# Kernel tuning notes

Hardware: AMD Instinct MI355X
Metric: run time of the kernel (lower is better)

## Reference

```python
import jax, jax.numpy as jnp
import numpy as np
from jax import lax

B, N, NPOINT, NSAMPLE = 16, 8192, 2048, 32
RADIUS = 0.45
D_FEAT = 64
MLP = (64, 64, 128)
EPS = 1e-5  # BatchNorm2d default eps


def setup_inputs() -> dict:
    key = jax.random.key(0)
    ks = jax.random.split(key, 8)
    inp = {
        "xyz": jax.random.uniform(ks[0], (B, 3, N), dtype=jnp.float32),
        "points": jax.random.normal(ks[1], (B, D_FEAT, N), dtype=jnp.float32),
    }
    dims = (3 + D_FEAT,) + MLP
    for i in range(len(MLP)):
        ci, co = dims[i], dims[i + 1]
        inp[f"W{i}"] = jax.random.normal(ks[2 + i], (co, ci), dtype=jnp.float32) / np.float32(np.sqrt(ci))
        inp[f"b{i}"] = jnp.zeros((co,), jnp.float32)
        inp[f"gamma{i}"] = jnp.ones((co,), jnp.float32)
        inp[f"beta{i}"] = jnp.zeros((co,), jnp.float32)
    return inp


def _fps(xyz_t, npoint):
    # farthest point sampling; xyz_t: [B, N, 3] -> [B, npoint] indices
    Bc, Nc, _ = xyz_t.shape

    def step(carry, _):
        distance, farthest = carry
        centroid = jnp.take_along_axis(xyz_t, farthest[:, None, None], axis=1)  # [B,1,3]
        d = jnp.sum((xyz_t - centroid) ** 2, axis=-1)  # [B,N]
        distance = jnp.minimum(distance, d)
        return (distance, jnp.argmax(distance, axis=-1)), farthest

    init = (jnp.full((Bc, Nc), 1e10, xyz_t.dtype), jnp.zeros((Bc,), jnp.int32))
    _, cents = lax.scan(step, init, None, length=npoint)
    return jnp.transpose(cents)  # [B, npoint]


def _gather(pts, idx):
    # pts: [B, N, C], idx: [B, ...] -> [B, ..., C]
    return jax.vmap(lambda p, i: p[i])(pts, idx)


def _forward(xyz, points, params):
    xyz_t = jnp.transpose(xyz, (0, 2, 1))     # [B,N,3]
    pts_t = jnp.transpose(points, (0, 2, 1))  # [B,N,D]

    fps_idx = _fps(xyz_t, NPOINT)
    new_xyz = _gather(xyz_t, fps_idx)         # [B,S,3]

    # ball query -- faithful to source: Euclidean DISTANCE compared vs radius**2
    d2 = (jnp.sum(new_xyz ** 2, -1)[:, :, None]
          + jnp.sum(xyz_t ** 2, -1)[:, None, :]
          - 2.0 * jnp.einsum('bsc,bnc->bsn', new_xyz, xyz_t))
    dist = jnp.sqrt(jnp.maximum(d2, 0.0))     # [B,S,N] == torch.cdist
    neg_vals, idx = lax.top_k(-dist, NSAMPLE)
    group_idx = jnp.where(-neg_vals < RADIUS ** 2, idx, 0)  # [B,S,K]

    grouped_xyz = _gather(xyz_t, group_idx) - new_xyz[:, :, None, :]  # [B,S,K,3]
    grouped_pts = _gather(pts_t, group_idx)                           # [B,S,K,D]
    feats = jnp.concatenate([grouped_xyz, grouped_pts], axis=-1)      # [B,S,K,3+D]

    # shared MLP: 1x1 conv + BatchNorm (training-mode batch stats) + ReLU
    for (W, b, g, be) in params:
        h = jnp.einsum('bskc,oc->bsko', feats, W) + b
        mean = jnp.mean(h, axis=(0, 1, 2))
        var = jnp.var(h, axis=(0, 1, 2))  # biased, like torch BN normalization
        feats = jax.nn.relu(g * (h - mean) * lax.rsqrt(var + EPS) + be)

    new_points = jnp.max(feats, axis=2)  # max over nsample -> [B,S,C_out]
    return jnp.transpose(new_xyz, (0, 2, 1)), jnp.transpose(new_points, (0, 2, 1))


def reference(xyz, points, W0, b0, gamma0, beta0, W1, b1, gamma1, beta1, W2, b2, gamma2, beta2):
    params = [(W0, b0, gamma0, beta0), (W1, b1, gamma1, beta1), (W2, b2, gamma2, beta2)]
    return _forward(xyz, points, params)
```

## Files before the change

### kernel.cpp

```cpp
#include <hip/hip_runtime.h>

#define B_ 16
#define N_ 8192
#define S_ 2048
#define K_ 32
#define EPSBN 1e-5
#define CAP 1024

#define OFF_PARTA    0ul
#define OFF_NEWXYZ   131072ul
#define OFF_GIDX     524288ul
#define OFF_Q1       4718592ul
#define OFF_C1       38273024ul
#define OFF_PART     46661632ul
#define OFF_AFF1     55050240ul
#define OFF_AFF2     55051264ul
#define OFF_AFF3     55052288ul
#define OFF_H3MAX    55053312ul
#define OFF_H3MIN    71830528ul

#define STG(row, c) ((row)*33 + ((row)>>5) + (c))

template<int CTRL, int RM>
__device__ __forceinline__ unsigned long long dppmove(unsigned long long x) {
    unsigned int lo = (unsigned int)x, hi = (unsigned int)(x >> 32);
    unsigned int lo2 = (unsigned int)__builtin_amdgcn_update_dpp((int)lo, (int)lo, CTRL, RM, 0xf, false);
    unsigned int hi2 = (unsigned int)__builtin_amdgcn_update_dpp((int)hi, (int)hi, CTRL, RM, 0xf, false);
    return ((unsigned long long)hi2 << 32) | lo2;
}
__device__ __forceinline__ unsigned long long wave_max_u64(unsigned long long x) {
    unsigned long long t;
    t = dppmove<0x111, 0xf>(x); x = (t > x) ? t : x;
    t = dppmove<0x112, 0xf>(x); x = (t > x) ? t : x;
    t = dppmove<0x114, 0xf>(x); x = (t > x) ? t : x;
    t = dppmove<0x118, 0xf>(x); x = (t > x) ? t : x;
    t = dppmove<0x142, 0xa>(x); x = (t > x) ? t : x;
    t = dppmove<0x143, 0xc>(x); x = (t > x) ? t : x;
    return x;
}
__device__ __forceinline__ unsigned long long wave_min_u64(unsigned long long x) {
    unsigned long long t;
    t = dppmove<0x111, 0xf>(x); x = (t < x) ? t : x;
    t = dppmove<0x112, 0xf>(x); x = (t < x) ? t : x;
    t = dppmove<0x114, 0xf>(x); x = (t < x) ? t : x;
    t = dppmove<0x118, 0xf>(x); x = (t < x) ? t : x;
    t = dppmove<0x142, 0xa>(x); x = (t < x) ? t : x;
    t = dppmove<0x143, 0xc>(x); x = (t < x) ? t : x;
    return x;
}

__global__ __launch_bounds__(512) void fps_kernel(const float* __restrict__ xyz,
                                                  const float* __restrict__ pts,
                                                  const float* __restrict__ W0,
                                                  const float* __restrict__ b0,
                                                  float* __restrict__ Q1,
                                                  float* __restrict__ nxyz,
                                                  float* __restrict__ out0) {
    __shared__ float xs[N_], ys[N_], zs[N_];
    __shared__ int farHist[S_];
    __shared__ unsigned long long kq[2][8];
    int tid = threadIdx.x;
    if (blockIdx.x >= 16) {
        int o = tid & 63, jj = tid >> 6;
        int blk = blockIdx.x - 16;
        int b = blk >> 10;
        int j = ((blk & 1023) << 3) + jj;
        const float* xb = xyz + (size_t)b * 3 * N_;
        const float* pb = pts + (size_t)b * 64 * N_;
        float acc = b0[o];
#pragma unroll
        for (int c = 0; c < 3; c++) acc += W0[o * 67 + c] * xb[c * N_ + j];
#pragma unroll 8
        for (int c = 0; c < 64; c++) acc += W0[o * 67 + 3 + c] * pb[c * N_ + j];
        Q1[(((size_t)b << 13) + j) * 64 + o] = acc;
        return;
    }
    int b = blockIdx.x;
    const float* xb = xyz + (size_t)b * 3 * N_;
    for (int i = tid; i < N_; i += 512) {
        xs[i] = xb[i]; ys[i] = xb[N_ + i]; zs[i] = xb[2 * N_ + i];
    }
    __syncthreads();
    float px[16], py[16], pz[16], d8[16];
#pragma unroll
    for (int k = 0; k < 16; k++) {
        int i = tid + k * 512;
        px[k] = xs[i]; py[k] = ys[i]; pz[k] = zs[i];
        d8[k] = 1e10f;
    }
    int far = 0;
    int w = tid >> 6;
    for (int t = 0; t < S_; t++) {
        if (tid == 0) farHist[t] = far;
        float cx = xs[far], cy = ys[far], cz = zs[far];
        float bv = -1.f; int bk = 0;
#pragma unroll
        for (int k = 0; k < 16; k++) {
            float dx = px[k] - cx, dy = py[k] - cy, dz = pz[k] - cz;
            float d = dx * dx + dy * dy + dz * dz;
            float dd = fminf(d8[k], d); d8[k] = dd;
            if (dd > bv) { bv = dd; bk = k; }
        }
        int bi = tid + bk * 512;
        unsigned long long kk = (((unsigned long long)__float_as_uint(bv)) << 32)
                              | (unsigned)(8191 - bi);
        kk = wave_max_u64(kk);
        int buf = t & 1;
        if ((tid & 63) == 63) kq[buf][w] = kk;
        __syncthreads();
        unsigned long long fk = kq[buf][0];
#pragma unroll
        for (int q = 1; q < 8; q++) { unsigned long long o = kq[buf][q]; fk = (o > fk) ? o : fk; }
        far = 8191 - (int)(fk & 0xffffffffull);
    }
    __syncthreads();
    for (int s = tid; s < S_; s += 512) {
        int idx = farHist[s];
        float x = xs[idx], y = ys[idx], z = zs[idx];
        int g = b * S_ + s;
        nxyz[g * 3 + 0] = x; nxyz[g * 3 + 1] = y; nxyz[g * 3 + 2] = z;
        out0[(b * 3 + 0) * S_ + s] = x;
        out0[(b * 3 + 1) * S_ + s] = y;
        out0[(b * 3 + 2) * S_ + s] = z;
    }
}

__global__ __launch_bounds__(64) void ball_kernel(const float* __restrict__ xyz,
                                                  const float* __restrict__ nxyz,
                                                  int* __restrict__ gidx) {
    __shared__ unsigned long long keys[CAP];
    __shared__ int cnt;
    int bs = blockIdx.x; int b = bs >> 11; int tid = threadIdx.x;
    const float* xb = xyz + (size_t)b * 3 * N_;
    float cx = nxyz[bs * 3 + 0], cy = nxyz[bs * 3 + 1], cz = nxyz[bs * 3 + 2];
    float csq = __fadd_rn(__fadd_rn(__fmul_rn(cx, cx), __fmul_rn(cy, cy)), __fmul_rn(cz, cz));
    const float R2F = (float)(0.45 * 0.45);
    if (tid == 0) cnt = 0;
    __syncthreads();
    for (int j = tid; j < N_; j += 64) {
        float qx = xb[j], qy = xb[N_ + j], qz = xb[2 * N_ + j];
        float psq = __fadd_rn(__fadd_rn(__fmul_rn(qx, qx), __fmul_rn(qy, qy)), __fmul_rn(qz, qz));
        float t = __fmul_rn(cx, qx);
        t = __fmaf_rn(cy, qy, t);
        t = __fmaf_rn(cz, qz, t);
        float d2 = __fsub_rn(__fadd_rn(csq, psq), __fadd_rn(t, t));
        float dist = __fsqrt_rn(fmaxf(d2, 0.0f));
        if (dist < R2F) {
            int p = atomicAdd(&cnt, 1);
            if (p < CAP) keys[p] = (((unsigned long long)__float_as_uint(dist)) << 32) | (unsigned)j;
        }
    }
    __syncthreads();
    int nc = cnt; if (nc > CAP) nc = CAP;
    for (int k = 0; k < K_; k++) {
        unsigned long long bk = ~0ull;
        for (int i = tid; i < nc; i += 64) {
            unsigned long long kv = keys[i];
            bk = (kv < bk) ? kv : bk;
        }
        bk = wave_min_u64(bk);
        unsigned int lo = (unsigned int)__builtin_amdgcn_readlane((int)(unsigned int)bk, 63);
        unsigned int hi = (unsigned int)__builtin_amdgcn_readlane((int)(unsigned int)(bk >> 32), 63);
        unsigned long long mk = ((unsigned long long)hi << 32) | lo;
        int j = 0;
        if (mk != ~0ull) {
            j = (int)(mk & 0xffffffffull);
            for (int i = tid; i < nc; i += 64)
                if (keys[i] == mk) keys[i] = ~0ull;
        }
        if (tid == 0) gidx[bs * K_ + k] = j;
    }
}

__global__ __launch_bounds__(256) void c1_kernel(const float* __restrict__ nxyz,
                                                 const float* __restrict__ W0,
                                                 float* __restrict__ C1) {
    int tid = threadIdx.x; int o = tid & 63, ss = tid >> 6;
    int gs = blockIdx.x * 4 + ss;
    float acc = 0.f;
#pragma unroll
    for (int c = 0; c < 3; c++) acc += W0[o * 67 + c] * nxyz[gs * 3 + c];
    C1[(size_t)gs * 64 + o] = acc;
}

__global__ __launch_bounds__(256) void stats1_kernel(const float* __restrict__ Q1,
                                                     const float* __restrict__ C1,
                                                     const int* __restrict__ gidx,
                                                     double* __restrict__ part) {
    __shared__ double ds1[4][64], ds2[4][64];
    int tid = threadIdx.x; int o = tid & 63, ll = tid >> 6;
    double s1 = 0, s2 = 0;
    for (int it = 0; it < 256; it++) {
        int slot = it * 4096 + blockIdx.x * 4 + ll;
        int b = slot >> 16; int r = slot & 65535; int s = r >> 5;
        int g = gidx[slot];
        float q = Q1[(((size_t)b << 13) + g) * 64 + o];
        float c = C1[((size_t)(b << 11) + s) * 64 + o];
        float h = q - c;
        s1 += h; s2 += (double)h * (double)h;
    }
    ds1[ll][o] = s1; ds2[ll][o] = s2;
    __syncthreads();
    if (tid < 64) {
        double a = 0, bb = 0;
        for (int l = 0; l < 4; l++) { a += ds1[l][tid]; bb += ds2[l][tid]; }
        part[blockIdx.x * 256 + tid * 2] = a;
        part[blockIdx.x * 256 + tid * 2 + 1] = bb;
    }
}

__global__ void stats_reduceA_kernel(const double* __restrict__ part, int nblocks,
                                     double* __restrict__ partA) {
    int per = nblocks >> 6;
    int a = blockIdx.x;
    int c = threadIdx.x;
    double s = 0;
    for (int k = 0; k < per; k++)
        s += part[((size_t)(a * per + k)) * 256 + c];
    partA[(size_t)a * 256 + c] = s;
}

__global__ void stats_reduce_kernel(const double* __restrict__ part, int nblocks, int C,
                                    const float* __restrict__ gamma, const float* __restrict__ beta,
                                    float* __restrict__ aff) {
    __shared__ double s1s[512], s2s[512];
    int tid = threadIdx.x;
    int q = tid / C; int o = tid - q * C;
    double s1 = 0, s2 = 0;
    for (int i = q; i < nblocks; i += 4) {
        s1 += part[(size_t)i * 256 + o * 2];
        s2 += part[(size_t)i * 256 + o * 2 + 1];
    }
    s1s[tid] = s1; s2s[tid] = s2;
    __syncthreads();
    if (tid < C) {
        double a1 = s1s[tid] + s1s[tid + C] + s1s[tid + 2 * C] + s1s[tid + 3 * C];
        double a2 = s2s[tid] + s2s[tid + C] + s2s[tid + 2 * C] + s2s[tid + 3 * C];
        const double cnt = 1048576.0;
        double mean = a1 / cnt;
        double var = a2 / cnt - mean * mean; if (var < 0) var = 0;
        double a = (double)gamma[tid] / sqrt(var + EPSBN);
        double c = (double)beta[tid] - a * mean;
        aff[tid] = (float)a; aff[C + tid] = (float)c;
    }
}

__global__ __launch_bounds__(256) void layer2_stats_kernel(const float* __restrict__ Q1,
                                                           const float* __restrict__ C1,
                                                           const int* __restrict__ gidx,
                                                           const float* __restrict__ aff1,
                                                           const float* __restrict__ W1,
                                                           const float* __restrict__ b1,
                                                           double* __restrict__ part) {
    __shared__ __align__(16) float Wl[64 * 64];
    __shared__ float stage[256 * 33 + 8];
    __shared__ float sA[64], sC[64], sB[64];
    __shared__ double r1[8][33], r2[8][33];
    int tid = threadIdx.x;
    for (int i = tid; i < 4096; i += 256) { int o = i >> 6, c = i & 63; Wl[c * 64 + o] = W1[i]; }
    if (tid < 64) { sA[tid] = aff1[tid]; sC[tid] = aff1[64 + tid]; sB[tid] = b1[tid]; }
    __syncthreads();
    int slot = blockIdx.x * 256 + tid;
    int b = slot >> 16; int r = slot & 65535; int s = r >> 5;
    int g = gidx[slot];
    float x[64];
    {
        const float4* qp4 = (const float4*)(Q1 + (((size_t)b << 13) + g) * 64);
        const float4* cp4 = (const float4*)(C1 + ((size_t)(b << 11) + s) * 64);
#pragma unroll
        for (int c4 = 0; c4 < 16; c4++) {
            float4 q = qp4[c4], cc = cp4[c4];
            int c = c4 * 4;
            x[c + 0] = fmaxf(0.f, sA[c + 0] * (q.x - cc.x) + sC[c + 0]);
            x[c + 1] = fmaxf(0.f, sA[c + 1] * (q.y - cc.y) + sC[c + 1]);
            x[c + 2] = fmaxf(0.f, sA[c + 2] * (q.z - cc.z) + sC[c + 2]);
            x[c + 3] = fmaxf(0.f, sA[c + 3] * (q.w - cc.w) + sC[c + 3]);
        }
    }
    const float4* Wl4 = (const float4*)Wl;
    for (int ch = 0; ch < 2; ch++) {
        float acc[32];
#pragma unroll
        for (int o = 0; o < 32; o++) acc[o] = sB[ch * 32 + o];
#pragma unroll
        for (int c = 0; c < 64; c++) {
            float xv = x[c];
#pragma unroll
            for (int og = 0; og < 8; og++) {
                float4 w = Wl4[c * 16 + ch * 8 + og];
                acc[og * 4 + 0] += w.x * xv; acc[og * 4 + 1] += w.y * xv;
                acc[og * 4 + 2] += w.z * xv; acc[og * 4 + 3] += w.w * xv;
            }
        }
#pragma unroll
        for (int o = 0; o < 32; o++) stage[STG(tid, o)] = acc[o];
        __syncthreads();
        int chn = tid & 31, rr = tid >> 5;
        double s1 = 0, s2 = 0;
        for (int row = rr * 32; row < rr * 32 + 32; row++) {
            float v = stage[STG(row, chn)];
            s1 += v; s2 += (double)v * (double)v;
        }
        r1[rr][chn] = s1; r2[rr][chn] = s2;
        __syncthreads();
        if (tid < 32) {
            double a = 0, bb = 0;
            for (int l = 0; l < 8; l++) { a += r1[l][tid]; bb += r2[l][tid]; }
            part[blockIdx.x * 256 + (ch * 32 + tid) * 2] = a;
            part[blockIdx.x * 256 + (ch * 32 + tid) * 2 + 1] = bb;
        }
        __syncthreads();
    }
}

__global__ __launch_bounds__(256) void layer3_kernel(const float* __restrict__ Q1,
                                                     const float* __restrict__ C1,
                                                     const int* __restrict__ gidx,
                                                     const float* __restrict__ aff1,
                                                     const float* __restrict__ aff2,
                                                     const float* __restrict__ W1,
                                                     const float* __restrict__ b1,
                                                     const float* __restrict__ W2,
                                                     const float* __restrict__ b2,
                                                     double* __restrict__ part,
                                                     float* __restrict__ h3max,
                                                     float* __restrict__ h3min) {
    __shared__ __align__(16) float Wl[64 * 128];
    __shared__ float stage[256 * 33 + 8];
    __shared__ float sA1[64], sC1[64], sB1[64], sA2[64], sC2[64], sB2[128];
    __shared__ double r1[8][33], r2[8][33];
    int tid = threadIdx.x;
    for (int i = tid; i < 4096; i += 256) { int o = i >> 6, c = i & 63; Wl[c * 64 + o] = W1[i]; }
    if (tid < 64) {
        sA1[tid] = aff1[tid]; sC1[tid] = aff1[64 + tid]; sB1[tid] = b1[tid];
        sA2[tid] = aff2[tid]; sC2[tid] = aff2[64 + tid];
    }
    __syncthreads();
    int slot = blockIdx.x * 256 + tid;
    int b = slot >> 16; int r = slot & 65535; int s = r >> 5;
    int g = gidx[slot];
    float x[64];
    {
        const float4* qp4 = (const float4*)(Q1 + (((size_t)b << 13) + g) * 64);
        const float4* cp4 = (const float4*)(C1 + ((size_t)(b << 11) + s) * 64);
#pragma unroll
        for (int c4 = 0; c4 < 16; c4++) {
            float4 q = qp4[c4], cc = cp4[c4];
            int c = c4 * 4;
            x[c + 0] = fmaxf(0.f, sA1[c + 0] * (q.x - cc.x) + sC1[c + 0]);
            x[c + 1] = fmaxf(0.f, sA1[c + 1] * (q.y - cc.y) + sC1[c + 1]);
            x[c + 2] = fmaxf(0.f, sA1[c + 2] * (q.z - cc.z) + sC1[c + 2]);
            x[c + 3] = fmaxf(0.f, sA1[c + 3] * (q.w - cc.w) + sC1[c + 3]);
        }
    }
    const float4* Wl4 = (const float4*)Wl;
    float x3[64];
    for (int ch = 0; ch < 2; ch++) {
        float acc[32];
#pragma unroll
        for (int o = 0; o < 32; o++) acc[o] = sB1[ch * 32 + o];
#pragma unroll
        for (int c = 0; c < 64; c++) {
            float xv = x[c];
#pragma unroll
            for (int og = 0; og < 8; og++) {
                float4 w = Wl4[c * 16 + ch * 8 + og];
                acc[og * 4 + 0] += w.x * xv; acc[og * 4 + 1] += w.y * xv;
                acc[og * 4 + 2] += w.z * xv; acc[og * 4 + 3] += w.w * xv;
            }
        }
#pragma unroll
        for (int o = 0; o < 32; o++) {
            int oo = ch * 32 + o;
            x3[oo] = fmaxf(0.f, sA2[oo] * acc[o] + sC2[oo]);
        }
    }
    __syncthreads();
    for (int i = tid; i < 8192; i += 256) { int o = i >> 6, c = i & 63; Wl[c * 128 + o] = W2[i]; }
    if (tid < 128) sB2[tid] = b2[tid];
    __syncthreads();
    for (int ch = 0; ch < 4; ch++) {
        float acc[32];
#pragma unroll
        for (int o = 0; o < 32; o++) acc[o] = sB2[ch * 32 + o];
#pragma unroll
        for (int c = 0; c < 64; c++) {
            float xv = x3[c];
#pragma unroll
            for (int og = 0; og < 8; og++) {
                float4 w = Wl4[c * 32 + ch * 8 + og];
                acc[og * 4 + 0] += w.x * xv; acc[og * 4 + 1] += w.y * xv;
                acc[og * 4 + 2] += w.z * xv; acc[og * 4 + 3] += w.w * xv;
            }
        }
#pragma unroll
        for (int o = 0; o < 32; o++) stage[STG(tid, o)] = acc[o];
        __syncthreads();
        int chn = tid & 31, rr = tid >> 5;
        double s1 = 0, s2 = 0;
        float mx = -3.402823466e38f, mn = 3.402823466e38f;
        for (int row = rr * 32; row < rr * 32 + 32; row++) {
            float v = stage[STG(row, chn)];
            s1 += v; s2 += (double)v * (double)v;
            mx = fmaxf(mx, v); mn = fminf(mn, v);
        }
        r1[rr][chn] = s1; r2[rr][chn] = s2;
        int gg = blockIdx.x * 8 + rr;
        int bb_ = gg >> 11, ss_ = gg & 2047;
        h3max[((size_t)bb_ * 128 + ch * 32 + chn) * 2048 + ss_] = mx;
        h3min[((size_t)bb_ * 128 + ch * 32 + chn) * 2048 + ss_] = mn;
        __syncthreads();
        if (tid < 32) {
            double a = 0, bb = 0;
            for (int l = 0; l < 8; l++) { a += r1[l][tid]; bb += r2[l][tid]; }
            part[blockIdx.x * 256 + (ch * 32 + tid) * 2] = a;
            part[blockIdx.x * 256 + (ch * 32 + tid) * 2 + 1] = bb;
        }
        __syncthreads();
    }
}

__global__ void final_kernel(const float* __restrict__ h3max, const float* __restrict__ h3min,
                             const float* __restrict__ aff3, float* __restrict__ out1) {
    int idx = blockIdx.x * 256 + threadIdx.x;
    int ch = (idx >> 11) & 127;
    float a = aff3[ch], cv = aff3[128 + ch];
    float v = (a >= 0.f) ? h3max[idx] : h3min[idx];
    out1[idx] = fmaxf(0.f, a * v + cv);
}

extern "C" void kernel_launch(void* const* d_in, const int* in_sizes, int n_in,
                              void* d_out, int out_size, void* d_ws, size_t ws_size,
                              hipStream_t stream) {
    (void)in_sizes; (void)n_in; (void)out_size; (void)ws_size;
    const float* xyz = (const float*)d_in[0];
    const float* pts = (const float*)d_in[1];
    const float* W0  = (const float*)d_in[2];
    const float* b0  = (const float*)d_in[3];
    const float* g0  = (const float*)d_in[4];
    const float* be0 = (const float*)d_in[5];
    const float* W1  = (const float*)d_in[6];
    const float* b1  = (const float*)d_in[7];
    const float* g1  = (const float*)d_in[8];
    const float* be1 = (const float*)d_in[9];
    const float* W2  = (const float*)d_in[10];
    const float* b2  = (const float*)d_in[11];
    const float* g2  = (const float*)d_in[12];
    const float* be2 = (const float*)d_in[13];

    char* ws = (char*)d_ws;
    double* partA  = (double*)(ws + OFF_PARTA);
    float*  nxyz   = (float*)(ws + OFF_NEWXYZ);
    int*    gidx   = (int*)(ws + OFF_GIDX);
    float*  Q1     = (float*)(ws + OFF_Q1);
    float*  C1b    = (float*)(ws + OFF_C1);
    double* part   = (double*)(ws + OFF_PART);
    float*  aff1   = (float*)(ws + OFF_AFF1);
    float*  aff2   = (float*)(ws + OFF_AFF2);
    float*  aff3   = (float*)(ws + OFF_AFF3);
    float*  h3mx   = (float*)(ws + OFF_H3MAX);
    float*  h3mn   = (float*)(ws + OFF_H3MIN);
    float*  out0   = (float*)d_out;
    float*  out1   = out0 + B_ * 3 * S_;

    fps_kernel<<<16 + 16384, 512, 0, stream>>>(xyz, pts, W0, b0, Q1, nxyz, out0);
    ball_kernel<<<B_ * S_, 64, 0, stream>>>(xyz, nxyz, gidx);
    c1_kernel<<<(B_ * S_) / 4, 256, 0, stream>>>(nxyz, W0, C1b);
    stats1_kernel<<<1024, 256, 0, stream>>>(Q1, C1b, gidx, part);
    stats_reduceA_kernel<<<64, 256, 0, stream>>>(part, 1024, partA);
    stats_reduce_kernel<<<1, 256, 0, stream>>>(partA, 64, 64, g0, be0, aff1);
    layer2_stats_kernel<<<4096, 256, 0, stream>>>(Q1, C1b, gidx, aff1, W1, b1, part);
    stats_reduceA_kernel<<<64, 256, 0, stream>>>(part, 4096, partA);
    stats_reduce_kernel<<<1, 256, 0, stream>>>(partA, 64, 64, g1, be1, aff2);
    layer3_kernel<<<4096, 256, 0, stream>>>(Q1, C1b, gidx, aff1, aff2, W1, b1, W2, b2,
                                            part, h3mx, h3mn);
    stats_reduceA_kernel<<<64, 256, 0, stream>>>(part, 4096, partA);
    stats_reduce_kernel<<<1, 512, 0, stream>>>(partA, 64, 128, g2, be2, aff3);
    final_kernel<<<(B_ * 128 * S_) / 256, 256, 0, stream>>>(h3mx, h3mn, aff3, out1);
}
```

Measured before the change: 3.573 ms.

## Use 256 FPS threads with 32 points each; process two rows per thread in MLP kernels

The farthest-point-sampling loop now runs on 4 waves instead of 8, each thread holding 32 points, which halves the cross-wave reduction work per iteration. The layer2 and layer3 MLP kernels each compute two sample rows per thread, so every weight read from LDS is used for two rows and the grid shrinks to 2048 blocks. The cost is higher register pressure (two 32-wide accumulator sets plus two 64-float inputs), which may cause spills or lower occupancy. There are also extra barriers in the stats staging.

```diff
diff --git a/kernel.cpp b/kernel.cpp
--- a/kernel.cpp
+++ b/kernel.cpp
@@ -58,7 +58,7 @@
                                                   float* __restrict__ out0) {
     __shared__ float xs[N_], ys[N_], zs[N_];
     __shared__ int farHist[S_];
-    __shared__ unsigned long long kq[2][8];
+    __shared__ unsigned long long kq[2][4];
     int tid = threadIdx.x;
     if (blockIdx.x >= 16) {
         int o = tid & 63, jj = tid >> 6;
@@ -81,37 +81,43 @@
         xs[i] = xb[i]; ys[i] = xb[N_ + i]; zs[i] = xb[2 * N_ + i];
     }
     __syncthreads();
-    float px[16], py[16], pz[16], d8[16];
-#pragma unroll
-    for (int k = 0; k < 16; k++) {
-        int i = tid + k * 512;
-        px[k] = xs[i]; py[k] = ys[i]; pz[k] = zs[i];
-        d8[k] = 1e10f;
+    float px[32], py[32], pz[32], d8[32];
+    if (tid < 256) {
+#pragma unroll
+        for (int k = 0; k < 32; k++) {
+            int i = tid + k * 256;
+            px[k] = xs[i]; py[k] = ys[i]; pz[k] = zs[i];
+            d8[k] = 1e10f;
+        }
     }
     int far = 0;
     int w = tid >> 6;
     for (int t = 0; t < S_; t++) {
-        if (tid == 0) farHist[t] = far;
-        float cx = xs[far], cy = ys[far], cz = zs[far];
-        float bv = -1.f; int bk = 0;
-#pragma unroll
-        for (int k = 0; k < 16; k++) {
-            float dx = px[k] - cx, dy = py[k] - cy, dz = pz[k] - cz;
-            float d = dx * dx + dy * dy + dz * dz;
-            float dd = fminf(d8[k], d); d8[k] = dd;
-            if (dd > bv) { bv = dd; bk = k; }
-        }
-        int bi = tid + bk * 512;
-        unsigned long long kk = (((unsigned long long)__float_as_uint(bv)) << 32)
-                              | (unsigned)(8191 - bi);
-        kk = wave_max_u64(kk);
-        int buf = t & 1;
-        if ((tid & 63) == 63) kq[buf][w] = kk;
-        __syncthreads();
-        unsigned long long fk = kq[buf][0];
-#pragma unroll
-        for (int q = 1; q < 8; q++) { unsigned long long o = kq[buf][q]; fk = (o > fk) ? o : fk; }
-        far = 8191 - (int)(fk & 0xffffffffull);
+        if (tid < 256) {
+            if (tid == 0) farHist[t] = far;
+            float cx = xs[far], cy = ys[far], cz = zs[far];
+            float bv = -1.f; int bk = 0;
+#pragma unroll
+            for (int k = 0; k < 32; k++) {
+                float dx = px[k] - cx, dy = py[k] - cy, dz = pz[k] - cz;
+                float d = dx * dx + dy * dy + dz * dz;
+                float dd = fminf(d8[k], d); d8[k] = dd;
+                if (dd > bv) { bv = dd; bk = k; }
+            }
+            int bi = tid + bk * 256;
+            unsigned long long kk = (((unsigned long long)__float_as_uint(bv)) << 32)
+                                  | (unsigned)(8191 - bi);
+            kk = wave_max_u64(kk);
+            if ((tid & 63) == 63) kq[t & 1][w] = kk;
+        }
+        __syncthreads();
+        if (tid < 256) {
+            int buf = t & 1;
+            unsigned long long fk = kq[buf][0];
+#pragma unroll
+            for (int q = 1; q < 4; q++) { unsigned long long o = kq[buf][q]; fk = (o > fk) ? o : fk; }
+            far = 8191 - (int)(fk & 0xffffffffull);
+        }
     }
     __syncthreads();
     for (int s = tid; s < S_; s += 512) {
@@ -260,43 +266,55 @@
     for (int i = tid; i < 4096; i += 256) { int o = i >> 6, c = i & 63; Wl[c * 64 + o] = W1[i]; }
     if (tid < 64) { sA[tid] = aff1[tid]; sC[tid] = aff1[64 + tid]; sB[tid] = b1[tid]; }
     __syncthreads();
-    int slot = blockIdx.x * 256 + tid;
-    int b = slot >> 16; int r = slot & 65535; int s = r >> 5;
-    int g = gidx[slot];
-    float x[64];
-    {
+    float xA[64], xB[64];
+#pragma unroll
+    for (int half = 0; half < 2; half++) {
+        int slot = blockIdx.x * 512 + half * 256 + tid;
+        int b = slot >> 16; int r = slot & 65535; int s = r >> 5;
+        int g = gidx[slot];
         const float4* qp4 = (const float4*)(Q1 + (((size_t)b << 13) + g) * 64);
         const float4* cp4 = (const float4*)(C1 + ((size_t)(b << 11) + s) * 64);
+        float* xd = half ? xB : xA;
 #pragma unroll
         for (int c4 = 0; c4 < 16; c4++) {
             float4 q = qp4[c4], cc = cp4[c4];
             int c = c4 * 4;
-            x[c + 0] = fmaxf(0.f, sA[c + 0] * (q.x - cc.x) + sC[c + 0]);
-            x[c + 1] = fmaxf(0.f, sA[c + 1] * (q.y - cc.y) + sC[c + 1]);
-            x[c + 2] = fmaxf(0.f, sA[c + 2] * (q.z - cc.z) + sC[c + 2]);
-            x[c + 3] = fmaxf(0.f, sA[c + 3] * (q.w - cc.w) + sC[c + 3]);
+            xd[c + 0] = fmaxf(0.f, sA[c + 0] * (q.x - cc.x) + sC[c + 0]);
+            xd[c + 1] = fmaxf(0.f, sA[c + 1] * (q.y - cc.y) + sC[c + 1]);
+            xd[c + 2] = fmaxf(0.f, sA[c + 2] * (q.z - cc.z) + sC[c + 2]);
+            xd[c + 3] = fmaxf(0.f, sA[c + 3] * (q.w - cc.w) + sC[c + 3]);
         }
     }
     const float4* Wl4 = (const float4*)Wl;
     for (int ch = 0; ch < 2; ch++) {
-        float acc[32];
-#pragma unroll
-        for (int o = 0; o < 32; o++) acc[o] = sB[ch * 32 + o];
+        float accA[32], accB[32];
+#pragma unroll
+        for (int o = 0; o < 32; o++) { accA[o] = sB[ch * 32 + o]; accB[o] = accA[o]; }
 #pragma unroll
         for (int c = 0; c < 64; c++) {
-            float xv = x[c];
+            float xa = xA[c], xb2 = xB[c];
 #pragma unroll
             for (int og = 0; og < 8; og++) {
                 float4 w = Wl4[c * 16 + ch * 8 + og];
-                acc[og * 4 + 0] += w.x * xv; acc[og * 4 + 1] += w.y * xv;
-                acc[og * 4 + 2] += w.z * xv; acc[og * 4 + 3] += w.w * xv;
+                accA[og * 4 + 0] += w.x * xa; accA[og * 4 + 1] += w.y * xa;
+                accA[og * 4 + 2] += w.z * xa; accA[og * 4 + 3] += w.w * xa;
+                accB[og * 4 + 0] += w.x * xb2; accB[og * 4 + 1] += w.y * xb2;
+                accB[og * 4 + 2] += w.z * xb2; accB[og * 4 + 3] += w.w * xb2;
             }
         }
-#pragma unroll
-        for (int o = 0; o < 32; o++) stage[STG(tid, o)] = acc[o];
-        __syncthreads();
         int chn = tid & 31, rr = tid >> 5;
         double s1 = 0, s2 = 0;
+#pragma unroll
+        for (int o = 0; o < 32; o++) stage[STG(tid, o)] = accA[o];
+        __syncthreads();
+        for (int row = rr * 32; row < rr * 32 + 32; row++) {
+            float v = stage[STG(row, chn)];
+            s1 += v; s2 += (double)v * (double)v;
+        }
+        __syncthreads();
+#pragma unroll
+        for (int o = 0; o < 32; o++) stage[STG(tid, o)] = accB[o];
+        __syncthreads();
         for (int row = rr * 32; row < rr * 32 + 32; row++) {
             float v = stage[STG(row, chn)];
             s1 += v; s2 += (double)v * (double)v;
@@ -336,11 +354,14 @@
         sA2[tid] = aff2[tid]; sC2[tid] = aff2[64 + tid];
     }
     __syncthreads();
-    int slot = blockIdx.x * 256 + tid;
-    int b = slot >> 16; int r = slot & 65535; int s = r >> 5;
-    int g = gidx[slot];
-    float x[64];
-    {
+    const float4* Wl4 = (const float4*)Wl;
+    float x3A[64], x3B[64];
+#pragma unroll
+    for (int half = 0; half < 2; half++) {
+        int slot = blockIdx.x * 512 + half * 256 + tid;
+        int b = slot >> 16; int r = slot & 65535; int s = r >> 5;
+        int g = gidx[slot];
+        float x[64];
         const float4* qp4 = (const float4*)(Q1 + (((size_t)b << 13) + g) * 64);
         const float4* cp4 = (const float4*)(C1 + ((size_t)(b << 11) + s) * 64);
 #pragma unroll
@@ -352,27 +373,26 @@
             x[c + 2] = fmaxf(0.f, sA1[c + 2] * (q.z - cc.z) + sC1[c + 2]);
             x[c + 3] = fmaxf(0.f, sA1[c + 3] * (q.w - cc.w) + sC1[c + 3]);
         }
-    }
-    const float4* Wl4 = (const float4*)Wl;
-    float x3[64];
-    for (int ch = 0; ch < 2; ch++) {
-        float acc[32];
-#pragma unroll
-        for (int o = 0; o < 32; o++) acc[o] = sB1[ch * 32 + o];
-#pragma unroll
-        for (int c = 0; c < 64; c++) {
-            float xv = x[c];
-#pragma unroll
-            for (int og = 0; og < 8; og++) {
-                float4 w = Wl4[c * 16 + ch * 8 + og];
-                acc[og * 4 + 0] += w.x * xv; acc[og * 4 + 1] += w.y * xv;
-                acc[og * 4 + 2] += w.z * xv; acc[og * 4 + 3] += w.w * xv;
+        float* x3 = half ? x3B : x3A;
+        for (int ch = 0; ch < 2; ch++) {
+            float acc[32];
+#pragma unroll
+            for (int o = 0; o < 32; o++) acc[o] = sB1[ch * 32 + o];
+#pragma unroll
+            for (int c = 0; c < 64; c++) {
+                float xv = x[c];
+#pragma unroll
+                for (int og = 0; og < 8; og++) {
+                    float4 w = Wl4[c * 16 + ch * 8 + og];
+                    acc[og * 4 + 0] += w.x * xv; acc[og * 4 + 1] += w.y * xv;
+                    acc[og * 4 + 2] += w.z * xv; acc[og * 4 + 3] += w.w * xv;
+                }
             }
-        }
-#pragma unroll
-        for (int o = 0; o < 32; o++) {
-            int oo = ch * 32 + o;
-            x3[oo] = fmaxf(0.f, sA2[oo] * acc[o] + sC2[oo]);
+#pragma unroll
+            for (int o = 0; o < 32; o++) {
+                int oo = ch * 32 + o;
+                x3[oo] = fmaxf(0.f, sA2[oo] * acc[o] + sC2[oo]);
+            }
         }
     }
     __syncthreads();
@@ -380,35 +400,41 @@
     if (tid < 128) sB2[tid] = b2[tid];
     __syncthreads();
     for (int ch = 0; ch < 4; ch++) {
-        float acc[32];
-#pragma unroll
-        for (int o = 0; o < 32; o++) acc[o] = sB2[ch * 32 + o];
+        float accA[32], accB[32];
+#pragma unroll
+        for (int o = 0; o < 32; o++) { accA[o] = sB2[ch * 32 + o]; accB[o] = accA[o]; }
 #pragma unroll
         for (int c = 0; c < 64; c++) {
-            float xv = x3[c];
+            float xa = x3A[c], xb2 = x3B[c];
 #pragma unroll
             for (int og = 0; og < 8; og++) {
                 float4 w = Wl4[c * 32 + ch * 8 + og];
-                acc[og * 4 + 0] += w.x * xv; acc[og * 4 + 1] += w.y * xv;
-                acc[og * 4 + 2] += w.z * xv; acc[og * 4 + 3] += w.w * xv;
+                accA[og * 4 + 0] += w.x * xa; accA[og * 4 + 1] += w.y * xa;
+                accA[og * 4 + 2] += w.z * xa; accA[og * 4 + 3] += w.w * xa;
+                accB[og * 4 + 0] += w.x * xb2; accB[og * 4 + 1] += w.y * xb2;
+                accB[og * 4 + 2] += w.z * xb2; accB[og * 4 + 3] += w.w * xb2;
             }
         }
-#pragma unroll
-        for (int o = 0; o < 32; o++) stage[STG(tid, o)] = acc[o];
-        __syncthreads();
         int chn = tid & 31, rr = tid >> 5;
         double s1 = 0, s2 = 0;
-        float mx = -3.402823466e38f, mn = 3.402823466e38f;
-        for (int row = rr * 32; row < rr * 32 + 32; row++) {
-            float v = stage[STG(row, chn)];
-            s1 += v; s2 += (double)v * (double)v;
-            mx = fmaxf(mx, v); mn = fminf(mn, v);
+#pragma unroll
+        for (int half = 0; half < 2; half++) {
+#pragma unroll
+            for (int o = 0; o < 32; o++) stage[STG(tid, o)] = half ? accB[o] : accA[o];
+            __syncthreads();
+            float mx = -3.402823466e38f, mn = 3.402823466e38f;
+            for (int row = rr * 32; row < rr * 32 + 32; row++) {
+                float v = stage[STG(row, chn)];
+                s1 += v; s2 += (double)v * (double)v;
+                mx = fmaxf(mx, v); mn = fminf(mn, v);
+            }
+            int gg = blockIdx.x * 16 + half * 8 + rr;
+            int bb_ = gg >> 11, ss_ = gg & 2047;
+            h3max[((size_t)bb_ * 128 + ch * 32 + chn) * 2048 + ss_] = mx;
+            h3min[((size_t)bb_ * 128 + ch * 32 + chn) * 2048 + ss_] = mn;
+            __syncthreads();
         }
         r1[rr][chn] = s1; r2[rr][chn] = s2;
-        int gg = blockIdx.x * 8 + rr;
-        int bb_ = gg >> 11, ss_ = gg & 2047;
-        h3max[((size_t)bb_ * 128 + ch * 32 + chn) * 2048 + ss_] = mx;
-        h3min[((size_t)bb_ * 128 + ch * 32 + chn) * 2048 + ss_] = mn;
         __syncthreads();
         if (tid < 32) {
             double a = 0, bb = 0;
@@ -469,12 +495,12 @@
     stats1_kernel<<<1024, 256, 0, stream>>>(Q1, C1b, gidx, part);
     stats_reduceA_kernel<<<64, 256, 0, stream>>>(part, 1024, partA);
     stats_reduce_kernel<<<1, 256, 0, stream>>>(partA, 64, 64, g0, be0, aff1);
-    layer2_stats_kernel<<<4096, 256, 0, stream>>>(Q1, C1b, gidx, aff1, W1, b1, part);
-    stats_reduceA_kernel<<<64, 256, 0, stream>>>(part, 4096, partA);
+    layer2_stats_kernel<<<2048, 256, 0, stream>>>(Q1, C1b, gidx, aff1, W1, b1, part);
+    stats_reduceA_kernel<<<64, 256, 0, stream>>>(part, 2048, partA);
     stats_reduce_kernel<<<1, 256, 0, stream>>>(partA, 64, 64, g1, be1, aff2);
-    layer3_kernel<<<4096, 256, 0, stream>>>(Q1, C1b, gidx, aff1, aff2, W1, b1, W2, b2,
+    layer3_kernel<<<2048, 256, 0, stream>>>(Q1, C1b, gidx, aff1, aff2, W1, b1, W2, b2,
                                             part, h3mx, h3mn);
-    stats_reduceA_kernel<<<64, 256, 0, stream>>>(part, 4096, partA);
+    stats_reduceA_kernel<<<64, 256, 0, stream>>>(part, 2048, partA);
     stats_reduce_kernel<<<1, 512, 0, stream>>>(partA, 64, 128, g2, be2, aff3);
     final_kernel<<<(B_ * 128 * S_) / 256, 256, 0, stream>>>(h3mx, h3mn, aff3, out1);
 }
```

Result: no change. 3.605 ms (+0.9%).
